# Optimization experiments

Measured on AMD Instinct MI355X. Metric: run time of the kernel, lower is better.

Reference implementation:

```python
import jax, jax.numpy as jnp
import numpy as np

B, S, D, H, DFF = 8, 1024, 1024, 16, 4096
HD = D // H
EPS_COS = 1e-8
EPS_LN = 1e-5


def setup_inputs() -> dict:
    key = jax.random.key(0)
    ks = jax.random.split(key, 12)
    inp = {
        "x": jax.random.normal(ks[0], (B, S, D), jnp.float32),
        "ln1_w": jnp.ones((D,), jnp.float32),
        "ln1_b": jnp.zeros((D,), jnp.float32),
        "in_proj_w": jax.random.normal(ks[1], (3 * D, D), jnp.float32) * 0.02,
        "in_proj_b": jnp.zeros((3 * D,), jnp.float32),
        "out_proj_w": jax.random.normal(ks[2], (D, D), jnp.float32) * 0.02,
        "out_proj_b": jnp.zeros((D,), jnp.float32),
        "ln2_w": jnp.ones((D,), jnp.float32),
        "ln2_b": jnp.zeros((D,), jnp.float32),
        "mu_weight": jax.random.uniform(ks[3], (DFF, D), jnp.float32, -1.0, 1.0) * (1.0 / np.sqrt(D)),
        "sigma_weight": jax.random.normal(ks[4], (DFF, D), jnp.float32) * 0.02,
        "gate_param": jnp.full((DFF,), 0.1, jnp.float32),
        "mu_bias": jnp.zeros((DFF,), jnp.float32),
        "ffn2_w": jax.random.normal(ks[5], (D, DFF), jnp.float32) * 0.02,
        "ffn2_b": jnp.zeros((D,), jnp.float32),
    }
    return inp


def _layernorm(x, w, b):
    mu = jnp.mean(x, axis=-1, keepdims=True)
    var = jnp.mean(jnp.square(x - mu), axis=-1, keepdims=True)
    return (x - mu) * jax.lax.rsqrt(var + EPS_LN) * w + b


def _mha_causal(h, in_proj_w, in_proj_b, out_proj_w, out_proj_b):
    # h: [B,S,D]; combined qkv projection as in torch nn.MultiheadAttention
    qkv = h @ in_proj_w.T + in_proj_b                      # [B,S,3D]
    q, k, v = jnp.split(qkv, 3, axis=-1)
    def heads(t):
        return t.reshape(B, S, H, HD).transpose(0, 2, 1, 3)  # [B,H,S,HD]
    q, k, v = heads(q), heads(k), heads(v)
    logits = jnp.einsum("bhqd,bhkd->bhqk", q, k) / jnp.sqrt(jnp.float32(HD))
    causal = jnp.tril(jnp.ones((S, S), bool))
    logits = jnp.where(causal, logits, jnp.float32(-jnp.inf))
    attn = jax.nn.softmax(logits, axis=-1)
    o = jnp.einsum("bhqk,bhkd->bhqd", attn, v)
    o = o.transpose(0, 2, 1, 3).reshape(B, S, D)
    return o @ out_proj_w.T + out_proj_b


def _moie_linear(xr, mu_weight, sigma_weight, gate_param, mu_bias):
    # xr: [N,D]. cosine similarity via GEMM + norm reductions (no (N,out,in) blowup)
    keys = mu_weight * jax.nn.softplus(sigma_weight)       # [DFF,D]
    dots = xr @ keys.T                                      # [N,DFF]
    xn = jnp.maximum(jnp.linalg.norm(xr, axis=-1, keepdims=True), EPS_COS)
    kn = jnp.maximum(jnp.linalg.norm(keys, axis=-1), EPS_COS)
    scores = dots / (xn * kn[None, :])                      # [N,DFF]
    weights = jax.nn.relu(scores - gate_param[None, :])
    comp = xr @ mu_weight.T + mu_bias                       # [N,DFF]
    masked = comp * weights
    return masked, scores


def reference(x, ln1_w, ln1_b, in_proj_w, in_proj_b, out_proj_w, out_proj_b,
              ln2_w, ln2_b, mu_weight, sigma_weight, gate_param, mu_bias,
              ffn2_w, ffn2_b):
    h = _layernorm(x, ln1_w, ln1_b)
    attn_out = _mha_causal(h, in_proj_w, in_proj_b, out_proj_w, out_proj_b)
    x = x + attn_out
    ffn_in = _layernorm(x, ln2_w, ln2_b)
    xr = ffn_in.reshape(-1, D)                              # [N,D]
    masked, scores = _moie_linear(xr, mu_weight, sigma_weight, gate_param, mu_bias)
    ffn1_out = masked.reshape(B, S, DFF)
    act = jax.nn.silu(ffn1_out)
    ffn2_out = act @ ffn2_w.T + ffn2_b
    x = x + ffn2_out
    return x, scores, masked
```

## Files before the change

### kernel.cpp

```cpp
#include <hip/hip_runtime.h>

typedef unsigned short u16;
typedef unsigned int u32;
typedef unsigned long long u64;
typedef __attribute__((ext_vector_type(8))) short short8;
typedef __attribute__((ext_vector_type(4))) float f32x4;

#define DEV static __device__ __forceinline__

#define DPPF(v, c) __int_as_float(__builtin_amdgcn_mov_dpp(__float_as_int(v), (c), 0xf, 0xf, true))

DEV u16 f2b(float f) {
  union { float f; u32 u; } a; a.f = f;
  u32 r = a.u + 0x7fffu + ((a.u >> 16) & 1u);
  return (u16)(r >> 16);
}

DEV f32x4 mfma16(short8 a, short8 b, f32x4 c) {
  return __builtin_amdgcn_mfma_f32_16x16x32_bf16(a, b, c, 0, 0, 0);
}

DEV void async16(const void* g, void* l) {
  __builtin_amdgcn_global_load_lds(
      (const __attribute__((address_space(1))) u32*)g,
      (__attribute__((address_space(3))) u32*)l, 16, 0, 0);
}

__global__ __launch_bounds__(256) void f2bf_multi(
    const float* __restrict__ s0, const float* __restrict__ s1,
    const float* __restrict__ s2, u16* __restrict__ dst) {
  const int stride = gridDim.x * 256;
  for (int i = blockIdx.x * 256 + threadIdx.x; i < 2097152; i += stride) {
    f32x4 v;
    if (i < 786432) v = ((const f32x4*)s0)[i];
    else if (i < 1048576) v = ((const f32x4*)s1)[i - 786432];
    else v = ((const f32x4*)s2)[i - 1048576];
    union { u64 q; u16 s[4]; } pk;
    pk.s[0] = f2b(v[0]); pk.s[1] = f2b(v[1]); pk.s[2] = f2b(v[2]); pk.s[3] = f2b(v[3]);
    ((u64*)dst)[i] = pk.q;
  }
}

__global__ __launch_bounds__(256) void prep_keys(
    const float* __restrict__ mu, const float* __restrict__ sg,
    u16* __restrict__ wcat, float* __restrict__ kn) {
  __shared__ float s1[4];
  const int row = blockIdx.x, tid = threadIdx.x, lane = tid & 63, wave = tid >> 6;
  const f32x4 m = *(const f32x4*)(mu + (size_t)row * 1024 + tid * 4);
  const f32x4 s = *(const f32x4*)(sg + (size_t)row * 1024 + tid * 4);
  float q = 0.f;
  union { u64 q; u16 s[4]; } pkk, pkm;
  #pragma unroll
  for (int j = 0; j < 4; ++j) {
    const float sp = (s[j] > 20.f) ? s[j] : log1pf(__expf(s[j]));
    const float k = m[j] * sp;
    q += k * k;
    pkk.s[j] = f2b(k);
    pkm.s[j] = f2b(m[j]);
  }
  *(u64*)(wcat + (size_t)row * 1024 + tid * 4) = pkk.q;
  *(u64*)(wcat + (size_t)(4096 + row) * 1024 + tid * 4) = pkm.q;
  #pragma unroll
  for (int d = 1; d < 64; d <<= 1) q += __shfl_xor(q, d);
  if (lane == 0) s1[wave] = q;
  __syncthreads();
  if (tid == 0) kn[row] = 1.0f / fmaxf(sqrtf(s1[0] + s1[1] + s1[2] + s1[3]), 1e-8f);
}

__global__ __launch_bounds__(256) void ln4_kernel(
    const float* __restrict__ x, const float* __restrict__ w,
    const float* __restrict__ b, u16* __restrict__ y, float* __restrict__ xn) {
  const int tid = threadIdx.x, lane = tid & 63, wave = tid >> 6;
  const int row = blockIdx.x * 4 + wave;
  const float* xr = x + (size_t)row * 1024;
  f32x4 xv[4];
  float s = 0.f, q = 0.f;
  #pragma unroll
  for (int j = 0; j < 4; ++j) {
    xv[j] = *(const f32x4*)(xr + j * 256 + lane * 4);
    #pragma unroll
    for (int u = 0; u < 4; ++u) { s += xv[j][u]; q += xv[j][u] * xv[j][u]; }
  }
  #pragma unroll
  for (int d = 1; d < 64; d <<= 1) { s += __shfl_xor(s, d); q += __shfl_xor(q, d); }
  const float mean = s * (1.f / 1024.f);
  const float inv = rsqrtf(q * (1.f / 1024.f) - mean * mean + 1e-5f);
  float qs = 0.f;
  #pragma unroll
  for (int j = 0; j < 4; ++j) {
    const f32x4 wv = *(const f32x4*)(w + j * 256 + lane * 4);
    const f32x4 bv = *(const f32x4*)(b + j * 256 + lane * 4);
    union { u64 q; u16 s[4]; } pk;
    #pragma unroll
    for (int u = 0; u < 4; ++u) {
      const float yv = (xv[j][u] - mean) * inv * wv[u] + bv[u];
      qs += yv * yv;
      pk.s[u] = f2b(yv);
    }
    *(u64*)(y + (size_t)row * 1024 + j * 256 + lane * 4) = pk.q;
  }
  if (xn) {
    #pragma unroll
    for (int d = 1; d < 64; d <<= 1) qs += __shfl_xor(qs, d);
    if (lane == 0) xn[row] = 1.0f / fmaxf(sqrtf(qs), 1e-8f);
  }
}

template<int MODE, int BM>
__global__ __launch_bounds__(512, 2) void gemm_bt(
    const u16* __restrict__ A, const u16* __restrict__ W,
    int M, int N, int K,
    const float* __restrict__ aux0, const float* __restrict__ aux1,
    float* __restrict__ fo0,
    u16* __restrict__ bo0, u16* __restrict__ bo1, u16* __restrict__ bo2) {
  constexpr int MF = BM / 32;
  constexpr int A_U16 = BM * 32;
  constexpr int STRIDE = A_U16 + 8192;
  constexpr int AISS = BM / 128;
  constexpr int LPT = AISS + 2;
  __shared__ __align__(16) u16 lds[3 * STRIDE];

  const int tid = threadIdx.x;
  const int lane = tid & 63, wave = tid >> 6;
  const int x = lane & 15, g = lane >> 4;
  const int wm = wave >> 2, wn = wave & 3;

  const int gx = N >> 8;
  const int nwg = gridDim.x;
  const int wg = ((int)blockIdx.x & 7) * (nwg >> 3) + ((int)blockIdx.x >> 3);
  const int by = wg / gx, bx = wg - by * gx;
  const int m0 = by * BM, n0 = bx * 256;

  const u16* srcA[AISS]; const u16* srcB[2];
  int dA[AISS], dB[2];
  #pragma unroll
  for (int i = 0; i < AISS; ++i) {
    const int rp = i * 64 + (tid >> 3);
    const int pre = (tid & 7) ^ (rp & 7);
    const int row = rp * 2 + (pre & 1), col = (pre >> 1) * 8;
    srcA[i] = A + (size_t)(m0 + row) * K + col;
    dA[i] = i * 4096 + tid * 8;
  }
  #pragma unroll
  for (int i = 0; i < 2; ++i) {
    const int rp = i * 64 + (tid >> 3);
    const int pre = (tid & 7) ^ (rp & 7);
    const int row = rp * 2 + (pre & 1), col = (pre >> 1) * 8;
    srcB[i] = W + (size_t)(n0 + row) * K + col;
    dB[i] = A_U16 + i * 4096 + tid * 8;
  }
  const int lane_off = (x >> 1) * 64 + (((2 * g + (x & 1)) ^ (x >> 1)) * 8);
  const int aoff = wm * (BM / 4) * 64 + lane_off;
  const int boff = A_U16 + wn * 2048 + lane_off;

  f32x4 acc[MF][4];
  #pragma unroll
  for (int f = 0; f < MF; ++f)
    #pragma unroll
    for (int j = 0; j < 4; ++j) acc[f][j] = (f32x4){0.f, 0.f, 0.f, 0.f};

  const int NT = K >> 5;
  auto stage = [&](int t, int b) {
    u16* buf = lds + b * STRIDE;
    const size_t ko = (size_t)t * 32;
    #pragma unroll
    for (int i = 0; i < AISS; ++i) async16(srcA[i] + ko, buf + dA[i]);
    #pragma unroll
    for (int i = 0; i < 2; ++i) async16(srcB[i] + ko, buf + dB[i]);
  };
  stage(0, 0);
  stage(1, 1);
  int br = 0, bs = 2;
  for (int t = 0; t < NT; ++t) {
    if (t < NT - 1)
      asm volatile("s_waitcnt vmcnt(%0)\n\ts_barrier" :: "n"(LPT) : "memory");
    else
      asm volatile("s_waitcnt vmcnt(0)\n\ts_barrier" ::: "memory");
    const u16* bufr = lds + br * STRIDE;
    short8 bfr[4], af[MF];
    #pragma unroll
    for (int j = 0; j < 4; ++j) bfr[j] = *(const short8*)(bufr + boff + j * 512);
    #pragma unroll
    for (int f = 0; f < MF; ++f) af[f] = *(const short8*)(bufr + aoff + f * 512);
    if (t + 2 < NT) stage(t + 2, bs);
    __builtin_amdgcn_s_setprio(1);
    #pragma unroll
    for (int f = 0; f < MF; ++f)
      #pragma unroll
      for (int j = 0; j < 4; ++j) acc[f][j] = mfma16(af[f], bfr[j], acc[f][j]);
    __builtin_amdgcn_s_setprio(0);
    br = (br == 2) ? 0 : br + 1;
    bs = (bs == 2) ? 0 : bs + 1;
  }

  const int col_base = n0 + wn * 64;
  const int row_base = m0 + wm * (BM / 2);
  #pragma unroll
  for (int f = 0; f < MF; ++f)
    #pragma unroll
    for (int j = 0; j < 4; ++j)
      #pragma unroll
      for (int r = 0; r < 4; ++r) {
        const int row = row_base + f * 16 + g * 4 + r;
        const int col = col_base + j * 16 + x;
        float v = acc[f][j][r];
        if constexpr (MODE == 0) {
          v += aux0[col];
          const int part = col >> 10, cc = col & 1023;
          const int hh = cc >> 6, dd = cc & 63;
          const size_t idx = ((size_t)((row >> 10) * 16 + hh) * 1024 + (row & 1023)) * 64 + dd;
          if (part == 0) bo0[idx] = f2b(v * 0.125f);
          else if (part == 1) bo1[idx] = f2b(v);
          else bo2[idx] = f2b(v);
        } else if constexpr (MODE == 1) {
          fo0[(size_t)row * 1024 + col] = v + aux0[col] + aux1[(size_t)row * 1024 + col];
        } else {
          __builtin_nontemporal_store(
              v + aux0[col] + aux1[(size_t)row * 1024 + col],
              &fo0[(size_t)row * 1024 + col]);
        }
      }
}

__global__ __launch_bounds__(512, 2) void moie_gemm(
    const u16* __restrict__ A, const u16* __restrict__ W,
    const float* __restrict__ xni, const float* __restrict__ kni,
    const float* __restrict__ mub, const float* __restrict__ gate,
    float* __restrict__ oscore, float* __restrict__ omask,
    u16* __restrict__ oact) {
  __shared__ __align__(16) u16 lds[4 * 16384];
  const int tid = threadIdx.x;
  const int lane = tid & 63, wave = tid >> 6;
  const int x = lane & 15, g = lane >> 4, h = x >> 1, pp = x & 1;
  const int wm = wave >> 2, wn = wave & 3;

  const int bid = (int)blockIdx.x;
  const int local = bid >> 3;
  const int by = (bid & 7) * 4 + (local & 3);
  const int bx = local >> 2;
  const int m0 = by * 256, n0 = bx * 128;

  const int rp0 = tid >> 3, j0 = tid & 7;
  const int prow = rp0 * 2 + (j0 & 1);
  const int pcol = (((j0 >> 1) ^ (rp0 & 3)) & 3) * 8;
  const u16* Asrc[2]; const u16* Bsrc[2];
  Asrc[0] = A + (size_t)(m0 + prow) * 1024 + pcol;
  Asrc[1] = A + (size_t)(m0 + 128 + prow) * 1024 + pcol;
  #pragma unroll
  for (int c = 0; c < 2; ++c) {
    const int rb = c * 128 + prow;
    const u16* base = (rb & 32) ? (W + (size_t)4096 * 1024) : W;
    Bsrc[c] = base + (size_t)(n0 + ((rb >> 6) << 5) + (rb & 31)) * 1024 + pcol;
  }
  const int dst0 = tid * 8;
  const int laneoff = h * 64 + (((2 * g + pp) ^ ((h & 3) << 1)) * 8);

  f32x4 acc[8][4];
  #pragma unroll
  for (int i = 0; i < 8; ++i)
    #pragma unroll
    for (int j = 0; j < 4; ++j) acc[i][j] = (f32x4){0.f, 0.f, 0.f, 0.f};

  auto stageA = [&](int t) {
    u16* dst = lds + (t & 3) * 16384 + dst0;
    const int ko = t * 32;
    async16(Asrc[0] + ko, dst);
    async16(Asrc[1] + ko, dst + 4096);
  };
  auto stageB = [&](int t) {
    u16* dst = lds + (t & 3) * 16384 + 8192 + dst0;
    const int ko = t * 32;
    async16(Bsrc[0] + ko, dst);
    async16(Bsrc[1] + ko, dst + 4096);
  };

  stageA(0); stageB(0); stageA(1); stageB(1); stageA(2); stageB(2);
  asm volatile("s_waitcnt vmcnt(8)\n\ts_barrier" ::: "memory");

  constexpr int NT = 32;
  for (int t = 0; t < NT; ++t) {
    const u16* bufA = lds + (t & 3) * 16384;
    const u16* bufB = bufA + 8192;
    short8 bf[4], af[8];
    #pragma unroll
    for (int j = 0; j < 4; ++j)
      bf[j] = *(const short8*)(bufB + wn * 2048 + j * 512 + laneoff);
    #pragma unroll
    for (int f = 0; f < 8; ++f)
      af[f] = *(const short8*)(bufA + wm * 4096 + f * 512 + laneoff);
    if (t + 3 < NT) { stageB(t + 3); stageA(t + 3); }
    __builtin_amdgcn_s_setprio(1);
    #pragma unroll
    for (int f = 0; f < 8; ++f)
      #pragma unroll
      for (int j = 0; j < 4; ++j) acc[f][j] = mfma16(af[f], bf[j], acc[f][j]);
    __builtin_amdgcn_s_setprio(0);
    if (t <= NT - 4)
      asm volatile("s_waitcnt vmcnt(8)\n\ts_barrier" ::: "memory");
    else if (t == NT - 3)
      asm volatile("s_waitcnt vmcnt(4)\n\ts_barrier" ::: "memory");
    else if (t == NT - 2)
      asm volatile("s_waitcnt vmcnt(0)\n\ts_barrier" ::: "memory");
  }

  #pragma unroll
  for (int i = 0; i < 8; ++i) {
    const int row = m0 + wm * 128 + i * 16 + g * 4;
    const f32x4 xv = *(const f32x4*)(xni + row);
    #pragma unroll
    for (int jj = 0; jj < 2; ++jj) {
      const int gcol = n0 + wn * 32 + jj * 16 + x;
      const float kv = kni[gcol], gt = gate[gcol], mb = mub[gcol];
      #pragma unroll
      for (int r = 0; r < 4; ++r) {
        const float s = acc[i][jj][r] * xv[r] * kv;
        const float comp = acc[i][jj + 2][r] + mb;
        const float mk = comp * fmaxf(s - gt, 0.f);
        oscore[(size_t)(row + r) * 4096 + gcol] = s;
        omask[(size_t)(row + r) * 4096 + gcol] = mk;
        oact[(size_t)(row + r) * 4096 + gcol] = f2b(mk / (1.f + __expf(-mk)));
      }
    }
  }
}

__global__ __launch_bounds__(256) void vtrans(const u16* __restrict__ v,
                                              u16* __restrict__ vt) {
  __shared__ u16 tl[64 * 66];
  const int bh = blockIdx.y, s0 = blockIdx.x * 64;
  const int tid = threadIdx.x;
  const int r8 = tid >> 3, c8 = tid & 7;
  #pragma unroll
  for (int p = 0; p < 2; ++p) {
    const int row = r8 + p * 32;
    *(short8*)&tl[row * 66 + c8 * 8] =
        *(const short8*)&v[((size_t)bh * 1024 + s0 + row) * 64 + c8 * 8];
  }
  __syncthreads();
  #pragma unroll
  for (int p = 0; p < 2; ++p) {
    const int d = r8 + p * 32;
    union { short8 v; u16 s[8]; } pk;
    #pragma unroll
    for (int j = 0; j < 8; ++j) pk.s[j] = tl[(c8 * 8 + j) * 66 + d];
    *(short8*)&vt[((size_t)bh * 64 + d) * 1024 + s0 + c8 * 8] = pk.v;
  }
}

__global__ __launch_bounds__(256) void attn_kernel(
    const u16* __restrict__ Q, const u16* __restrict__ Kg,
    const u16* __restrict__ Vtg, u16* __restrict__ O) {
  __shared__ __align__(16) u16 Kb[2][4096];
  __shared__ __align__(16) u16 Vb[2][4096];
  __shared__ __align__(16) u16 Pl[4][1024];
  const int bh = blockIdx.x;
  const int qt = blockIdx.y;
  const int tid = threadIdx.x, lane = tid & 63, wave = tid >> 6;
  const int x = lane & 15, g = lane >> 4;
  const u16* Qb = Q + (size_t)bh * 1024 * 64;
  const int qbase = qt * 64 + wave * 16;
  const short8 qf0 = *(const short8*)&Qb[(qbase + x) * 64 + g * 8];
  const short8 qf1 = *(const short8*)&Qb[(qbase + x) * 64 + 32 + g * 8];

  const int rp = tid >> 3, j0 = tid & 7;
  const int prow = rp * 2 + (j0 & 1);
  const int pcol = (((j0 >> 1) ^ (rp & 3)) & 3) * 8;
  const u16* srcK = Kg + (size_t)bh * 65536 + (size_t)prow * 64 + pcol;
  const u16* srcV = Vtg + (size_t)(bh * 64 + prow) * 1024 + pcol;
  const int dst0 = tid * 8;
  const int h = x >> 1, pq = x & 1;
  const int laneoff = h * 64 + (((2 * g + pq) ^ ((h & 3) << 1)) * 8);

  float mrun[4], lrun[4];
  f32x4 oacc[4];
  #pragma unroll
  for (int r = 0; r < 4; ++r) { mrun[r] = -1e30f; lrun[r] = 0.f; }
  #pragma unroll
  for (int d = 0; d < 4; ++d) oacc[d] = (f32x4){0.f, 0.f, 0.f, 0.f};

  auto stage = [&](int t) {
    u16* kd = Kb[t & 1] + dst0;
    u16* vd = Vb[t & 1] + dst0;
    const u16* ks = srcK + t * 4096;
    const u16* vs = srcV + t * 64;
    async16(ks, kd);        async16(ks + 32, kd + 2048);
    async16(vs, vd);        async16(vs + 32, vd + 2048);
  };
  stage(0);
  asm volatile("s_waitcnt vmcnt(0)\n\ts_barrier" ::: "memory");

  for (int t = 0; t <= qt; ++t) {
    const u16* kb = Kb[t & 1];
    const u16* vb = Vb[t & 1];
    if (t < qt) stage(t + 1);

    float sc[4][4];
    #pragma unroll
    for (int nb = 0; nb < 4; ++nb) {
      f32x4 a = (f32x4){0.f, 0.f, 0.f, 0.f};
      const short8 kf0 = *(const short8*)(kb + nb * 512 + laneoff);
      const short8 kf1 = *(const short8*)(kb + 2048 + nb * 512 + laneoff);
      a = mfma16(qf0, kf0, a);
      a = mfma16(qf1, kf1, a);
      #pragma unroll
      for (int r = 0; r < 4; ++r) sc[nb][r] = a[r];
    }
    if (t == qt) {
      #pragma unroll
      for (int nb = 0; nb < 4; ++nb)
        #pragma unroll
        for (int r = 0; r < 4; ++r)
          if (t * 64 + nb * 16 + x > qbase + g * 4 + r) sc[nb][r] = -1e30f;
    }
    float mnew[4], psum[4], scl[4];
    #pragma unroll
    for (int r = 0; r < 4; ++r) {
      float mx = fmaxf(fmaxf(sc[0][r], sc[1][r]), fmaxf(sc[2][r], sc[3][r]));
      mx = fmaxf(mx, DPPF(mx, 0xB1));
      mx = fmaxf(mx, DPPF(mx, 0x4E));
      mx = fmaxf(mx, DPPF(mx, 0x124));
      mx = fmaxf(mx, DPPF(mx, 0x128));
      mnew[r] = fmaxf(mrun[r], mx);
      scl[r] = __expf(mrun[r] - mnew[r]);
      mrun[r] = mnew[r];
      psum[r] = 0.f;
    }
    float p[4][4];
    #pragma unroll
    for (int nb = 0; nb < 4; ++nb)
      #pragma unroll
      for (int r = 0; r < 4; ++r) {
        p[nb][r] = __expf(sc[nb][r] - mnew[r]);
        psum[r] += p[nb][r];
      }
    #pragma unroll
    for (int r = 0; r < 4; ++r) {
      psum[r] += DPPF(psum[r], 0xB1);
      psum[r] += DPPF(psum[r], 0x4E);
      psum[r] += DPPF(psum[r], 0x124);
      psum[r] += DPPF(psum[r], 0x128);
      lrun[r] = lrun[r] * scl[r] + psum[r];
      #pragma unroll
      for (int db = 0; db < 4; ++db) oacc[db][r] *= scl[r];
    }
    u16* Pw = Pl[wave];
    #pragma unroll
    for (int nb = 0; nb < 4; ++nb) {
      const int half = nb >> 1;
      #pragma unroll
      for (int r = 0; r < 4; ++r) {
        const int qr = g * 4 + r;
        const int col5 = (nb & 1) * 16 + x;
        const int c8 = col5 >> 3, c7 = col5 & 7;
        const int rq = qr >> 1;
        const int jq = (qr & 1) | ((c8 ^ (rq & 3)) << 1);
        Pw[half * 512 + rq * 64 + jq * 8 + c7] = f2b(p[nb][r]);
      }
    }
    const short8 pf0 = *(const short8*)(Pw + laneoff);
    const short8 pf1 = *(const short8*)(Pw + 512 + laneoff);
    #pragma unroll
    for (int db = 0; db < 4; ++db) {
      const short8 vf0 = *(const short8*)(vb + db * 512 + laneoff);
      const short8 vf1 = *(const short8*)(vb + 2048 + db * 512 + laneoff);
      oacc[db] = mfma16(pf0, vf0, oacc[db]);
      oacc[db] = mfma16(pf1, vf1, oacc[db]);
    }
    if (t < qt)
      asm volatile("s_waitcnt vmcnt(0)\n\ts_barrier" ::: "memory");
  }
  const int b = bh >> 4, hh = bh & 15;
  #pragma unroll
  for (int db = 0; db < 4; ++db)
    #pragma unroll
    for (int r = 0; r < 4; ++r) {
      const int qrow = qbase + g * 4 + r;
      O[((size_t)(b * 1024 + qrow)) * 1024 + hh * 64 + db * 16 + x] = f2b(oacc[db][r] / lrun[r]);
    }
}

extern "C" void kernel_launch(void* const* d_in, const int* in_sizes, int n_in,
                              void* d_out, int out_size, void* d_ws, size_t ws_size,
                              hipStream_t stream) {
  const float* x    = (const float*)d_in[0];
  const float* ln1w = (const float*)d_in[1];
  const float* ln1b = (const float*)d_in[2];
  const float* wip  = (const float*)d_in[3];
  const float* bip  = (const float*)d_in[4];
  const float* wop  = (const float*)d_in[5];
  const float* bop  = (const float*)d_in[6];
  const float* ln2w = (const float*)d_in[7];
  const float* ln2b = (const float*)d_in[8];
  const float* muw  = (const float*)d_in[9];
  const float* sgw  = (const float*)d_in[10];
  const float* gate = (const float*)d_in[11];
  const float* mub  = (const float*)d_in[12];
  const float* wf2  = (const float*)d_in[13];
  const float* bf2  = (const float*)d_in[14];

  float* out_x = (float*)d_out;
  float* out_scores = out_x + (size_t)8192 * 1024;
  float* out_masked = out_scores + (size_t)8192 * 4096;

  char* ws = (char*)d_ws;
  size_t off = 0;
  auto alloc = [&](size_t n) { char* p = ws + off; off += (n + 255) & ~(size_t)255; return p; };
  u16* h_bf    = (u16*)alloc((size_t)8192 * 1024 * 2);
  u16* q_bf    = (u16*)alloc((size_t)8192 * 1024 * 2);
  u16* k_bf    = (u16*)alloc((size_t)8192 * 1024 * 2);
  u16* v_bf    = (u16*)alloc((size_t)8192 * 1024 * 2);
  u16* vt_bf   = (u16*)alloc((size_t)8192 * 1024 * 2);
  u16* o_bf    = (u16*)alloc((size_t)8192 * 1024 * 2);
  float* x_res = (float*)alloc((size_t)8192 * 1024 * 4);
  u16* xr_bf   = (u16*)alloc((size_t)8192 * 1024 * 2);
  float* xn    = (float*)alloc((size_t)8192 * 4);
  float* kn    = (float*)alloc((size_t)4096 * 4);
  u16* wcat    = (u16*)alloc((size_t)8192 * 1024 * 2);
  u16* wip_b   = (u16*)alloc((size_t)3072 * 1024 * 2);
  u16* wop_b   = (u16*)alloc((size_t)1024 * 1024 * 2);
  u16* wf2_b   = (u16*)alloc((size_t)1024 * 4096 * 2);
  u16* act_bf  = (u16*)alloc((size_t)8192 * 4096 * 2);

  f2bf_multi<<<2048, 256, 0, stream>>>(wip, wop, wf2, wip_b);
  prep_keys<<<4096, 256, 0, stream>>>(muw, sgw, wcat, kn);
  ln4_kernel<<<2048, 256, 0, stream>>>(x, ln1w, ln1b, h_bf, nullptr);
  gemm_bt<0, 128><<<768, 512, 0, stream>>>(h_bf, wip_b, 8192, 3072, 1024,
      bip, nullptr, nullptr, q_bf, k_bf, v_bf);
  vtrans<<<dim3(16, 128), 256, 0, stream>>>(v_bf, vt_bf);
  attn_kernel<<<dim3(128, 16), 256, 0, stream>>>(q_bf, k_bf, vt_bf, o_bf);
  gemm_bt<1, 128><<<256, 512, 0, stream>>>(o_bf, wop_b, 8192, 1024, 1024,
      bop, x, x_res, nullptr, nullptr, nullptr);
  ln4_kernel<<<2048, 256, 0, stream>>>(x_res, ln2w, ln2b, xr_bf, xn);
  moie_gemm<<<1024, 512, 0, stream>>>(xr_bf, wcat, xn, kn, mub, gate,
      out_scores, out_masked, act_bf);
  gemm_bt<3, 128><<<256, 512, 0, stream>>>(act_bf, wf2_b, 8192, 1024, 4096,
      bf2, x_res, out_x, nullptr, nullptr, nullptr);
}
```

Measured before the change: 500.5 us.

## Shrink MoIE GEMM tile to 128x128 with triple-buffered LDS and higher occupancy

The fused MoIE GEMM drops from 256x128 output tiles with a 4-stage LDS ring to 128x128 tiles with a 3-stage ring, and the grid doubles to 2048 blocks. The launch bound rises to 4 blocks per CU, and the wait/barrier now sits at the top of each k-step instead of the bottom. The aim is more resident waves and better latency hiding on the 8192x8192 dual-weight GEMM. The cost is less operand reuse per tile, so more global/L2 traffic for the A and weight tiles, plus more register pressure at the new occupancy target.

```diff
diff --git a/kernel.cpp b/kernel.cpp
--- a/kernel.cpp
+++ b/kernel.cpp
@@ -222,90 +222,88 @@
       }
 }
 
-__global__ __launch_bounds__(512, 2) void moie_gemm(
+__global__ __launch_bounds__(512, 4) void moie_gemm(
     const u16* __restrict__ A, const u16* __restrict__ W,
     const float* __restrict__ xni, const float* __restrict__ kni,
     const float* __restrict__ mub, const float* __restrict__ gate,
     float* __restrict__ oscore, float* __restrict__ omask,
     u16* __restrict__ oact) {
-  __shared__ __align__(16) u16 lds[4 * 16384];
+  constexpr int STRIDE = 12288;
+  __shared__ __align__(16) u16 lds[3 * STRIDE];
   const int tid = threadIdx.x;
   const int lane = tid & 63, wave = tid >> 6;
-  const int x = lane & 15, g = lane >> 4, h = x >> 1, pp = x & 1;
+  const int x = lane & 15, g = lane >> 4;
   const int wm = wave >> 2, wn = wave & 3;
 
   const int bid = (int)blockIdx.x;
   const int local = bid >> 3;
-  const int by = (bid & 7) * 4 + (local & 3);
-  const int bx = local >> 2;
-  const int m0 = by * 256, n0 = bx * 128;
-
-  const int rp0 = tid >> 3, j0 = tid & 7;
-  const int prow = rp0 * 2 + (j0 & 1);
-  const int pcol = (((j0 >> 1) ^ (rp0 & 3)) & 3) * 8;
-  const u16* Asrc[2]; const u16* Bsrc[2];
-  Asrc[0] = A + (size_t)(m0 + prow) * 1024 + pcol;
-  Asrc[1] = A + (size_t)(m0 + 128 + prow) * 1024 + pcol;
-  #pragma unroll
-  for (int c = 0; c < 2; ++c) {
-    const int rb = c * 128 + prow;
+  const int by = (bid & 7) * 8 + (local & 7);
+  const int bx = local >> 3;
+  const int m0 = by * 128, n0 = bx * 128;
+
+  const u16* srcA;
+  const u16* srcB[2];
+  {
+    const int rp = tid >> 3;
+    const int pre = (tid & 7) ^ (rp & 7);
+    const int row = rp * 2 + (pre & 1), col = (pre >> 1) * 8;
+    srcA = A + (size_t)(m0 + row) * 1024 + col;
+  }
+  #pragma unroll
+  for (int i = 0; i < 2; ++i) {
+    const int rp = i * 64 + (tid >> 3);
+    const int pre = (tid & 7) ^ (rp & 7);
+    const int rb = rp * 2 + (pre & 1), col = (pre >> 1) * 8;
     const u16* base = (rb & 32) ? (W + (size_t)4096 * 1024) : W;
-    Bsrc[c] = base + (size_t)(n0 + ((rb >> 6) << 5) + (rb & 31)) * 1024 + pcol;
-  }
-  const int dst0 = tid * 8;
-  const int laneoff = h * 64 + (((2 * g + pp) ^ ((h & 3) << 1)) * 8);
-
-  f32x4 acc[8][4];
-  #pragma unroll
-  for (int i = 0; i < 8; ++i)
-    #pragma unroll
-    for (int j = 0; j < 4; ++j) acc[i][j] = (f32x4){0.f, 0.f, 0.f, 0.f};
-
-  auto stageA = [&](int t) {
-    u16* dst = lds + (t & 3) * 16384 + dst0;
-    const int ko = t * 32;
-    async16(Asrc[0] + ko, dst);
-    async16(Asrc[1] + ko, dst + 4096);
+    srcB[i] = base + (size_t)(n0 + ((rb >> 6) << 5) + (rb & 31)) * 1024 + col;
+  }
+  const int dB0 = 4096 + tid * 8, dB1 = 8192 + tid * 8;
+  const int lane_off = (x >> 1) * 64 + (((2 * g + (x & 1)) ^ (x >> 1)) * 8);
+  const int aoff = wm * 2048 + lane_off;
+  const int boff = 4096 + wn * 2048 + lane_off;
+
+  f32x4 acc[4][4];
+  #pragma unroll
+  for (int f = 0; f < 4; ++f)
+    #pragma unroll
+    for (int j = 0; j < 4; ++j) acc[f][j] = (f32x4){0.f, 0.f, 0.f, 0.f};
+
+  constexpr int NT = 32;
+  auto stage = [&](int t, int b) {
+    u16* buf = lds + b * STRIDE;
+    const size_t ko = (size_t)t * 32;
+    async16(srcA + ko, buf + tid * 8);
+    async16(srcB[0] + ko, buf + dB0);
+    async16(srcB[1] + ko, buf + dB1);
   };
-  auto stageB = [&](int t) {
-    u16* dst = lds + (t & 3) * 16384 + 8192 + dst0;
-    const int ko = t * 32;
-    async16(Bsrc[0] + ko, dst);
-    async16(Bsrc[1] + ko, dst + 4096);
-  };
-
-  stageA(0); stageB(0); stageA(1); stageB(1); stageA(2); stageB(2);
-  asm volatile("s_waitcnt vmcnt(8)\n\ts_barrier" ::: "memory");
-
-  constexpr int NT = 32;
+  stage(0, 0);
+  stage(1, 1);
+  int br = 0, bs = 2;
   for (int t = 0; t < NT; ++t) {
-    const u16* bufA = lds + (t & 3) * 16384;
-    const u16* bufB = bufA + 8192;
-    short8 bf[4], af[8];
-    #pragma unroll
-    for (int j = 0; j < 4; ++j)
-      bf[j] = *(const short8*)(bufB + wn * 2048 + j * 512 + laneoff);
-    #pragma unroll
-    for (int f = 0; f < 8; ++f)
-      af[f] = *(const short8*)(bufA + wm * 4096 + f * 512 + laneoff);
-    if (t + 3 < NT) { stageB(t + 3); stageA(t + 3); }
+    if (t < NT - 1)
+      asm volatile("s_waitcnt vmcnt(3)\n\ts_barrier" ::: "memory");
+    else
+      asm volatile("s_waitcnt vmcnt(0)\n\ts_barrier" ::: "memory");
+    const u16* bufr = lds + br * STRIDE;
+    short8 bfr[4], af[4];
+    #pragma unroll
+    for (int j = 0; j < 4; ++j) bfr[j] = *(const short8*)(bufr + boff + j * 512);
+    #pragma unroll
+    for (int f = 0; f < 4; ++f) af[f] = *(const short8*)(bufr + aoff + f * 512);
+    if (t + 2 < NT) stage(t + 2, bs);
     __builtin_amdgcn_s_setprio(1);
     #pragma unroll
-    for (int f = 0; f < 8; ++f)
-      #pragma unroll
-      for (int j = 0; j < 4; ++j) acc[f][j] = mfma16(af[f], bf[j], acc[f][j]);
+    for (int f = 0; f < 4; ++f)
+      #pragma unroll
+      for (int j = 0; j < 4; ++j) acc[f][j] = mfma16(af[f], bfr[j], acc[f][j]);
     __builtin_amdgcn_s_setprio(0);
-    if (t <= NT - 4)
-      asm volatile("s_waitcnt vmcnt(8)\n\ts_barrier" ::: "memory");
-    else if (t == NT - 3)
-      asm volatile("s_waitcnt vmcnt(4)\n\ts_barrier" ::: "memory");
-    else if (t == NT - 2)
-      asm volatile("s_waitcnt vmcnt(0)\n\ts_barrier" ::: "memory");
-  }
-
-  #pragma unroll
-  for (int i = 0; i < 8; ++i) {
-    const int row = m0 + wm * 128 + i * 16 + g * 4;
+    br = (br == 2) ? 0 : br + 1;
+    bs = (bs == 2) ? 0 : bs + 1;
+  }
+
+  #pragma unroll
+  for (int f = 0; f < 4; ++f) {
+    const int row = m0 + wm * 64 + f * 16 + g * 4;
     const f32x4 xv = *(const f32x4*)(xni + row);
     #pragma unroll
     for (int jj = 0; jj < 2; ++jj) {
@@ -313,8 +311,8 @@
       const float kv = kni[gcol], gt = gate[gcol], mb = mub[gcol];
       #pragma unroll
       for (int r = 0; r < 4; ++r) {
-        const float s = acc[i][jj][r] * xv[r] * kv;
-        const float comp = acc[i][jj + 2][r] + mb;
+        const float s = acc[f][jj][r] * xv[r] * kv;
+        const float comp = acc[f][jj + 2][r] + mb;
         const float mk = comp * fmaxf(s - gt, 0.f);
         oscore[(size_t)(row + r) * 4096 + gcol] = s;
         omask[(size_t)(row + r) * 4096 + gcol] = mk;
@@ -531,7 +529,7 @@
   gemm_bt<1, 128><<<256, 512, 0, stream>>>(o_bf, wop_b, 8192, 1024, 1024,
       bop, x, x_res, nullptr, nullptr, nullptr);
   ln4_kernel<<<2048, 256, 0, stream>>>(x_res, ln2w, ln2b, xr_bf, xn);
-  moie_gemm<<<1024, 512, 0, stream>>>(xr_bf, wcat, xn, kn, mub, gate,
+  moie_gemm<<<2048, 512, 0, stream>>>(xr_bf, wcat, xn, kn, mub, gate,
       out_scores, out_masked, act_bf);
   gemm_bt<3, 128><<<256, 512, 0, stream>>>(act_bf, wf2_b, 8192, 1024, 4096,
       bf2, x_res, out_x, nullptr, nullptr, nullptr);
```

Result: slower. 517.2 us (+3.3%).

## Fuse prologue kernels into one launch and reverse attention q-tile order

Applied to the files above, without the earlier changes.

Merges the weight fp32-to-bf16 conversion, key preparation, and first LayerNorm into one kernel, with blocks dispatched by block-index range. This removes two launches and lets the three independent memory-bound jobs run concurrently on the GPU. Separately, the attention kernel now processes query tiles in reverse order so the longest causal tiles are scheduled first, reducing tail imbalance. The LayerNorm branch inlines the variance formula, which is assumed to match the original ln4 kernel.

```diff
diff --git a/kernel.cpp b/kernel.cpp
--- a/kernel.cpp
+++ b/kernel.cpp
@@ -26,45 +26,74 @@
       (__attribute__((address_space(3))) u32*)l, 16, 0, 0);
 }
 
-__global__ __launch_bounds__(256) void f2bf_multi(
-    const float* __restrict__ s0, const float* __restrict__ s1,
-    const float* __restrict__ s2, u16* __restrict__ dst) {
-  const int stride = gridDim.x * 256;
-  for (int i = blockIdx.x * 256 + threadIdx.x; i < 2097152; i += stride) {
-    f32x4 v;
-    if (i < 786432) v = ((const f32x4*)s0)[i];
-    else if (i < 1048576) v = ((const f32x4*)s1)[i - 786432];
-    else v = ((const f32x4*)s2)[i - 1048576];
-    union { u64 q; u16 s[4]; } pk;
-    pk.s[0] = f2b(v[0]); pk.s[1] = f2b(v[1]); pk.s[2] = f2b(v[2]); pk.s[3] = f2b(v[3]);
-    ((u64*)dst)[i] = pk.q;
-  }
-}
-
-__global__ __launch_bounds__(256) void prep_keys(
+__global__ __launch_bounds__(256) void prologue_k(
+    const float* __restrict__ s0, const float* __restrict__ s1f,
+    const float* __restrict__ s2, u16* __restrict__ wdst,
     const float* __restrict__ mu, const float* __restrict__ sg,
-    u16* __restrict__ wcat, float* __restrict__ kn) {
-  __shared__ float s1[4];
-  const int row = blockIdx.x, tid = threadIdx.x, lane = tid & 63, wave = tid >> 6;
-  const f32x4 m = *(const f32x4*)(mu + (size_t)row * 1024 + tid * 4);
-  const f32x4 s = *(const f32x4*)(sg + (size_t)row * 1024 + tid * 4);
-  float q = 0.f;
-  union { u64 q; u16 s[4]; } pkk, pkm;
-  #pragma unroll
-  for (int j = 0; j < 4; ++j) {
-    const float sp = (s[j] > 20.f) ? s[j] : log1pf(__expf(s[j]));
-    const float k = m[j] * sp;
-    q += k * k;
-    pkk.s[j] = f2b(k);
-    pkm.s[j] = f2b(m[j]);
-  }
-  *(u64*)(wcat + (size_t)row * 1024 + tid * 4) = pkk.q;
-  *(u64*)(wcat + (size_t)(4096 + row) * 1024 + tid * 4) = pkm.q;
-  #pragma unroll
-  for (int d = 1; d < 64; d <<= 1) q += __shfl_xor(q, d);
-  if (lane == 0) s1[wave] = q;
-  __syncthreads();
-  if (tid == 0) kn[row] = 1.0f / fmaxf(sqrtf(s1[0] + s1[1] + s1[2] + s1[3]), 1e-8f);
+    u16* __restrict__ wcat, float* __restrict__ kn,
+    const float* __restrict__ x, const float* __restrict__ lw,
+    const float* __restrict__ lb, u16* __restrict__ y) {
+  __shared__ float sred[4];
+  const int bid = (int)blockIdx.x;
+  const int tid = threadIdx.x, lane = tid & 63, wave = tid >> 6;
+  if (bid < 2048) {
+    const int stride = 2048 * 256;
+    for (int i = bid * 256 + tid; i < 2097152; i += stride) {
+      f32x4 v;
+      if (i < 786432) v = ((const f32x4*)s0)[i];
+      else if (i < 1048576) v = ((const f32x4*)s1f)[i - 786432];
+      else v = ((const f32x4*)s2)[i - 1048576];
+      union { u64 q; u16 s[4]; } pk;
+      pk.s[0] = f2b(v[0]); pk.s[1] = f2b(v[1]); pk.s[2] = f2b(v[2]); pk.s[3] = f2b(v[3]);
+      ((u64*)wdst)[i] = pk.q;
+    }
+  } else if (bid < 6144) {
+    const int row = bid - 2048;
+    const f32x4 m = *(const f32x4*)(mu + (size_t)row * 1024 + tid * 4);
+    const f32x4 s = *(const f32x4*)(sg + (size_t)row * 1024 + tid * 4);
+    float q = 0.f;
+    union { u64 q; u16 s[4]; } pkk, pkm;
+    #pragma unroll
+    for (int j = 0; j < 4; ++j) {
+      const float sp = (s[j] > 20.f) ? s[j] : log1pf(__expf(s[j]));
+      const float k = m[j] * sp;
+      q += k * k;
+      pkk.s[j] = f2b(k);
+      pkm.s[j] = f2b(m[j]);
+    }
+    *(u64*)(wcat + (size_t)row * 1024 + tid * 4) = pkk.q;
+    *(u64*)(wcat + (size_t)(4096 + row) * 1024 + tid * 4) = pkm.q;
+    #pragma unroll
+    for (int d = 1; d < 64; d <<= 1) q += __shfl_xor(q, d);
+    if (lane == 0) sred[wave] = q;
+    __syncthreads();
+    if (tid == 0) kn[row] = 1.0f / fmaxf(sqrtf(sred[0] + sred[1] + sred[2] + sred[3]), 1e-8f);
+  } else {
+    const int row = (bid - 6144) * 4 + wave;
+    const float* xr = x + (size_t)row * 1024;
+    f32x4 xv[4];
+    float s = 0.f, q = 0.f;
+    #pragma unroll
+    for (int j = 0; j < 4; ++j) {
+      xv[j] = *(const f32x4*)(xr + j * 256 + lane * 4);
+      #pragma unroll
+      for (int u = 0; u < 4; ++u) { s += xv[j][u]; q += xv[j][u] * xv[j][u]; }
+    }
+    #pragma unroll
+    for (int d = 1; d < 64; d <<= 1) { s += __shfl_xor(s, d); q += __shfl_xor(q, d); }
+    const float mean = s * (1.f / 1024.f);
+    const float inv = rsqrtf(q * (1.f / 1024.f) - mean * mean + 1e-5f);
+    #pragma unroll
+    for (int j = 0; j < 4; ++j) {
+      const f32x4 wv = *(const f32x4*)(lw + j * 256 + lane * 4);
+      const f32x4 bv = *(const f32x4*)(lb + j * 256 + lane * 4);
+      union { u64 q; u16 s[4]; } pk;
+      #pragma unroll
+      for (int u = 0; u < 4; ++u)
+        pk.s[u] = f2b((xv[j][u] - mean) * inv * wv[u] + bv[u]);
+      *(u64*)(y + (size_t)row * 1024 + j * 256 + lane * 4) = pk.q;
+    }
+  }
 }
 
 __global__ __launch_bounds__(256) void ln4_kernel(
@@ -354,7 +383,7 @@
   __shared__ __align__(16) u16 Vb[2][4096];
   __shared__ __align__(16) u16 Pl[4][1024];
   const int bh = blockIdx.x;
-  const int qt = blockIdx.y;
+  const int qt = 15 - (int)blockIdx.y;
   const int tid = threadIdx.x, lane = tid & 63, wave = tid >> 6;
   const int x = lane & 15, g = lane >> 4;
   const u16* Qb = Q + (size_t)bh * 1024 * 64;
@@ -521,9 +550,8 @@
   u16* wf2_b   = (u16*)alloc((size_t)1024 * 4096 * 2);
   u16* act_bf  = (u16*)alloc((size_t)8192 * 4096 * 2);
 
-  f2bf_multi<<<2048, 256, 0, stream>>>(wip, wop, wf2, wip_b);
-  prep_keys<<<4096, 256, 0, stream>>>(muw, sgw, wcat, kn);
-  ln4_kernel<<<2048, 256, 0, stream>>>(x, ln1w, ln1b, h_bf, nullptr);
+  prologue_k<<<8192, 256, 0, stream>>>(wip, wop, wf2, wip_b,
+      muw, sgw, wcat, kn, x, ln1w, ln1b, h_bf);
   gemm_bt<0, 128><<<768, 512, 0, stream>>>(h_bf, wip_b, 8192, 3072, 1024,
       bip, nullptr, nullptr, q_bf, k_bf, v_bf);
   vtrans<<<dim3(16, 128), 256, 0, stream>>>(v_bf, vt_bf);
```

After: 491.1 us. Within noise of the previous version (-1.9%).
